# Kernel optimization log

Measured on AMD Instinct MI355X. Metric: run time of the kernel, lower is better.

The kernel has to match this reference:

```python
import jax, jax.numpy as jnp
import numpy as np

H = 16   # num_heads
D = 16   # key_dim == output_dim (required by the module's reshape)
F = 64   # input feature dim


def setup_inputs() -> dict:
    key = jax.random.key(0)
    ks = jax.random.split(key, 8)
    B, N, Kn = 4, 4096, 32
    scale = 1.0 / np.sqrt(F)
    return {
        "inp": jax.random.normal(ks[0], (B, N, Kn, F), dtype=jnp.float32),
        "query": jax.random.normal(ks[1], (B, N, F), dtype=jnp.float32),
        "Wq": jax.random.normal(ks[2], (F, H * D), dtype=jnp.float32) * scale,
        "bq": jnp.zeros((H * D,), dtype=jnp.float32),
        "Wk": jax.random.normal(ks[3], (F, H * D), dtype=jnp.float32) * scale,
        "bk": jnp.zeros((H * D,), dtype=jnp.float32),
        "Wv": jax.random.normal(ks[4], (F, H * D), dtype=jnp.float32) * scale,
        "bv": jnp.zeros((H * D,), dtype=jnp.float32),
    }


def reference(inp, query, Wq, bq, Wk, bk, Wv, bv):
    B, N, Kn, _ = inp.shape
    # Dense projections
    Q = query @ Wq + bq                    # [B, N, H*D]
    K = inp @ Wk + bk                      # [B, N, Kn, H*D]
    V = inp @ Wv + bv                      # [B, N, Kn, H*D]
    # Faithful reshape (plain reshape of last dims, as in the TF code)
    Q = Q.reshape(B, N, H, 1, D)           # query broadcast axis of size 1
    K = K.reshape(B, N, H, Kn, D)
    V = V.reshape(B, N, H, Kn, D)
    # scaled dot-product attention per point over its Kn neighbors
    w = jnp.einsum('bnhqd,bnhkd->bnhqk', Q, K) / jnp.sqrt(jnp.float32(D))
    w = jax.nn.softmax(w, axis=-1)         # [B, N, H, 1, Kn]
    out = jnp.einsum('bnhqk,bnhkd->bnhqd', w, V)  # [B, N, H, 1, D]
    return out.reshape(B, N, H * D)
```

## Files before the change

### kernel.cpp

```cpp
#include <hip/hip_runtime.h>

#define KN 32
#define FF 64
#define CC 256
#define KSTR 260
#define VST 36
#define VTOFF (KN * KSTR)
#define NITER 16
#define QSTRIDE 264
#define WSTRIDE 36


typedef __attribute__((ext_vector_type(8)))  short bf16x8;
typedef __attribute__((ext_vector_type(16))) float f32x16;
typedef __attribute__((ext_vector_type(4)))  float f32x4;

__device__ inline unsigned short f2bf(float f) {
    union { float f; unsigned u; } v; v.f = f;
    unsigned u = v.u + 0x7fffu + ((v.u >> 16) & 1u);
    return (unsigned short)(u >> 16);
}
__device__ inline unsigned cvt_pk_bf16(float a, float b) {
    unsigned r;
    asm("v_cvt_pk_bf16_f32 %0, %1, %2" : "=v"(r) : "v"(a), "v"(b));
    return r;
}
__device__ inline bf16x8 pack8(float4 a, float4 b) {
    union { bf16x8 v; unsigned u[4]; } r;
    r.u[0] = cvt_pk_bf16(a.x, a.y);  r.u[1] = cvt_pk_bf16(a.z, a.w);
    r.u[2] = cvt_pk_bf16(b.x, b.y);  r.u[3] = cvt_pk_bf16(b.z, b.w);
    return r.v;
}

__device__ inline void lds_barrier() {
    asm volatile("s_waitcnt lgkmcnt(0)" ::: "memory");
    __builtin_amdgcn_s_barrier();
}

__global__ __launch_bounds__(256, 2)
void attn_one(const float* __restrict__ inp,
              const float* __restrict__ query,
              const float* __restrict__ Wq,
              const float* __restrict__ bq,
              const float* __restrict__ Wk,
              const float* __restrict__ bk,
              const float* __restrict__ Wv,
              const float* __restrict__ bv,
              float* __restrict__ out, int nPoints)
{
    __shared__ float kvS[KN * KSTR + CC * VST];
    __shared__ unsigned short qAllS[NITER * QSTRIDE];
    __shared__ float wS[16 * WSTRIDE];

    const int tid  = threadIdx.x;
    const int wave = tid >> 6;
    const int L    = tid & 63;
    const int Lm   = L & 31;
    const int Lh   = L >> 5;
    const int h    = tid >> 4;
    const int d    = tid & 15;
    const int bid  = blockIdx.x;
    const int grid = gridDim.x;

    float* qIn = kvS;
    {
        const int i  = tid >> 4;
        const int f4 = (tid & 15) * 4;
        const int p  = bid + i * grid;
        if (p < nPoints)
            *(float4*)(qIn + i * 68 + f4) =
                *(const float4*)(query + (size_t)p * FF + f4);
    }

    float4 pf[8];
    {
        const float* arow = inp + (size_t)bid * (KN * FF) + Lm * FF + Lh * 8;
#pragma unroll
        for (int s = 0; s < 4; ++s) {
            pf[2 * s]     = *(const float4*)(arow + s * 16);
            pf[2 * s + 1] = *(const float4*)(arow + s * 16 + 4);
        }
    }

    bf16x8 Bf[4][4];
#pragma unroll
    for (int t = 0; t < 4; ++t) {
        const float* W  = (t < 2) ? Wk : Wv;
        const int ch    = (2 * wave + (t & 1)) * 32 + Lm;
#pragma unroll
        for (int s = 0; s < 4; ++s) {
            union { bf16x8 v; unsigned u[4]; } r;
#pragma unroll
            for (int jj = 0; jj < 4; ++jj) {
                const int f = s * 16 + Lh * 8 + 2 * jj;
                r.u[jj] = cvt_pk_bf16(W[(size_t)f * CC + ch], W[(size_t)(f + 1) * CC + ch]);
            }
            Bf[t][s] = r.v;
        }
    }
    float biasV[2];
    biasV[0] = bv[(2 * wave + 0) * 32 + Lm];
    biasV[1] = bv[(2 * wave + 1) * 32 + Lm];
    float4 bkK[2][4];
#pragma unroll
    for (int t = 0; t < 2; ++t)
#pragma unroll
        for (int g = 0; g < 4; ++g)
            bkK[t][g] = *(const float4*)(bk + (2 * wave + t) * 32 + 8 * g + 4 * Lh);

    const int nq = L & 15;
    const int kq = (L >> 4) * 8;
    bf16x8 Bq[4][2];
    float  bqv[4];
#pragma unroll
    for (int tt = 0; tt < 4; ++tt) {
        const int ch = wave * 64 + tt * 16 + nq;
        bqv[tt] = bq[ch];
#pragma unroll
        for (int s = 0; s < 2; ++s) {
            union { bf16x8 v; unsigned u[4]; } r;
#pragma unroll
            for (int jj = 0; jj < 4; ++jj) {
                const int f = s * 32 + kq + 2 * jj;
                r.u[jj] = cvt_pk_bf16(Wq[(size_t)f * CC + ch], Wq[(size_t)(f + 1) * CC + ch]);
            }
            Bq[tt][s] = r.v;
        }
    }

    __syncthreads();

    {
        bf16x8 Aq[2];
        const int im = L & 15;
#pragma unroll
        for (int s = 0; s < 2; ++s) {
            const float* qr = qIn + im * 68 + s * 32 + kq;
            Aq[s] = pack8(*(const float4*)qr, *(const float4*)(qr + 4));
        }
#pragma unroll
        for (int tt = 0; tt < 4; ++tt) {
            f32x4 qa = {bqv[tt], bqv[tt], bqv[tt], bqv[tt]};
#pragma unroll
            for (int s = 0; s < 2; ++s)
                qa = __builtin_amdgcn_mfma_f32_16x16x32_bf16(Aq[s], Bq[tt][s], qa, 0, 0, 0);
            const int ch = wave * 64 + tt * 16 + nq;
#pragma unroll
            for (int r = 0; r < 4; ++r) {
                const int ip = (L >> 4) * 4 + r;
                qAllS[ip * QSTRIDE + ch] = f2bf(qa[r] * 0.25f);
            }
        }
    }
    __syncthreads();

    const int sR = d & 7;
    const int j0 = 2 * h + (d >> 3);

    for (int it = 0, p = bid; p < nPoints; ++it, p += grid) {
        bf16x8 Af[4];
#pragma unroll
        for (int s = 0; s < 4; ++s) Af[s] = pack8(pf[2 * s], pf[2 * s + 1]);

        const int pn = p + grid;
        if (pn < nPoints) {
            const float* arow = inp + (size_t)pn * (KN * FF) + Lm * FF + Lh * 8;
#pragma unroll
            for (int s = 0; s < 4; ++s) {
                pf[2 * s]     = *(const float4*)(arow + s * 16);
                pf[2 * s + 1] = *(const float4*)(arow + s * 16 + 4);
            }
        }

        f32x16 acc[4];
#pragma unroll
        for (int t = 0; t < 2; ++t)
#pragma unroll
            for (int g = 0; g < 4; ++g)
#pragma unroll
                for (int e = 0; e < 4; ++e) acc[t][4 * g + e] = bkK[t][g][e];
#pragma unroll
        for (int t = 2; t < 4; ++t)
#pragma unroll
            for (int r = 0; r < 16; ++r) acc[t][r] = biasV[t - 2];

#pragma unroll
        for (int s = 0; s < 4; ++s) {
#pragma unroll
            for (int t = 0; t < 2; ++t)
                acc[t] = __builtin_amdgcn_mfma_f32_32x32x16_bf16(Bf[t][s], Af[s], acc[t], 0, 0, 0);
#pragma unroll
            for (int t = 2; t < 4; ++t)
                acc[t] = __builtin_amdgcn_mfma_f32_32x32x16_bf16(Af[s], Bf[t][s], acc[t], 0, 0, 0);
        }

#pragma unroll
        for (int t = 0; t < 2; ++t) {
            float* kr = kvS + Lm * KSTR + (2 * wave + t) * 32 + 4 * Lh;
#pragma unroll
            for (int g = 0; g < 4; ++g) {
                float4 vw = {acc[t][4 * g], acc[t][4 * g + 1], acc[t][4 * g + 2], acc[t][4 * g + 3]};
                *(float4*)(kr + 8 * g) = vw;
            }
        }
#pragma unroll
        for (int t = 2; t < 4; ++t) {
            const int col = (2 * wave + (t & 1)) * 32 + Lm;
            float* vr = kvS + VTOFF + col * VST + 4 * Lh;
#pragma unroll
            for (int g = 0; g < 4; ++g) {
                float4 vw = {acc[t][4 * g], acc[t][4 * g + 1], acc[t][4 * g + 2], acc[t][4 * g + 3]};
                *(float4*)(vr + 8 * g) = vw;
            }
        }

        const unsigned short* qp = qAllS + it * QSTRIDE + h * 16;
        uint4 qA = *(const uint4*)qp;
        uint4 qB = *(const uint4*)(qp + 8);

        lds_barrier();

        const float* kb = kvS + j0 * KSTR + sR * 32;
        float4 ck[8];
#pragma unroll
        for (int w = 0; w < 8; ++w)
            ck[w] = *(const float4*)(kb + 4 * w);

        union { uint4 v; unsigned u[4]; } ua, ub;
        ua.v = qA;  ub.v = qB;
        float qv[16];
#pragma unroll
        for (int j = 0; j < 4; ++j) {
            qv[2 * j]     = __uint_as_float(ua.u[j] << 16);
            qv[2 * j + 1] = __uint_as_float(ua.u[j] & 0xffff0000u);
            qv[8 + 2 * j]     = __uint_as_float(ub.u[j] << 16);
            qv[8 + 2 * j + 1] = __uint_as_float(ub.u[j] & 0xffff0000u);
        }

        float l0a = 0.f, l0b = 0.f, l1a = 0.f, l1b = 0.f;
#pragma unroll
        for (int i = 0; i < 16; i += 2) {
            l0a = fmaf(qv[i],     ck[i >> 2][i & 3],             l0a);
            l0b = fmaf(qv[i + 1], ck[(i + 1) >> 2][(i + 1) & 3], l0b);
            l1a = fmaf(qv[i],     ck[4 + (i >> 2)][i & 3],             l1a);
            l1b = fmaf(qv[i + 1], ck[4 + ((i + 1) >> 2)][(i + 1) & 3], l1b);
        }
        const float l0 = l0a + l0b;
        const float l1 = l1a + l1b;

        float m = fmaxf(l0, l1);
        m = fmaxf(m, __shfl_xor(m, 1));
        m = fmaxf(m, __shfl_xor(m, 2));
        m = fmaxf(m, __shfl_xor(m, 4));
        m = fmaxf(m, __shfl_xor(m, 8));
        float e0 = __expf(l0 - m), e1 = __expf(l1 - m);
        float s2 = e0 + e1;
        s2 += __shfl_xor(s2, 1);
        s2 += __shfl_xor(s2, 2);
        s2 += __shfl_xor(s2, 4);
        s2 += __shfl_xor(s2, 8);
        const float inv = 1.0f / s2;
        *(float2*)(wS + h * WSTRIDE + 2 * d) = make_float2(e0 * inv, e1 * inv);
        __builtin_amdgcn_wave_barrier();

        float4 wv[8];
#pragma unroll
        for (int g = 0; g < 8; ++g)
            wv[g] = *(const float4*)(wS + h * WSTRIDE + 4 * g);

        const float* Vb = kvS + VTOFF + d * VST + 2 * h;
        float o0 = 0.f, o1 = 0.f, o2 = 0.f, o3 = 0.f;
#pragma unroll
        for (int mI = 0; mI < 16; mI += 2) {
            const float2 va = *(const float2*)(Vb + (size_t)(16 * mI) * VST);
            const float2 vb = *(const float2*)(Vb + (size_t)(16 * (mI + 1)) * VST);
            o0 = fmaf(wv[mI >> 2][mI & 3],             va.x, o0);
            o1 = fmaf(wv[4 + (mI >> 2)][mI & 3],       va.y, o1);
            o2 = fmaf(wv[(mI + 1) >> 2][(mI + 1) & 3],       vb.x, o2);
            o3 = fmaf(wv[4 + ((mI + 1) >> 2)][(mI + 1) & 3], vb.y, o3);
        }
        out[(size_t)p * CC + tid] = (o0 + o1) + (o2 + o3);

        lds_barrier();
    }
}

extern "C" void kernel_launch(void* const* d_in, const int* in_sizes, int n_in,
                              void* d_out, int out_size, void* d_ws, size_t ws_size,
                              hipStream_t stream) {
    const float* inp   = (const float*)d_in[0];
    const float* query = (const float*)d_in[1];
    const float* Wq    = (const float*)d_in[2];
    const float* bq    = (const float*)d_in[3];
    const float* Wk    = (const float*)d_in[4];
    const float* bk    = (const float*)d_in[5];
    const float* Wv    = (const float*)d_in[6];
    const float* bv    = (const float*)d_in[7];
    float* out = (float*)d_out;

    const int nPoints = in_sizes[0] / (KN * FF);
    const int grid    = (nPoints + NITER - 1) / NITER;

    attn_one<<<grid, 256, 0, stream>>>(inp, query, Wq, bq, Wk, bk, Wv, bv,
                                       out, nPoints);
}
```

Measured before the change: 254.5 us.

## Store K/V tiles as bf16 in LDS, raise occupancy, prioritize MFMA

Projected K and V are now packed to bf16 before being written to shared memory, and the attention loop unpacks them on read. This halves the LDS footprint and the LDS traffic per point. The launch bound rises from 2 to 3 blocks per CU to use the freed LDS. The MFMA block is also wrapped in s_setprio to favour matrix issue. The risks are extra bf16 rounding error on K and V, and register pressure at the higher occupancy target.

```diff
diff --git a/kernel.cpp b/kernel.cpp
--- a/kernel.cpp
+++ b/kernel.cpp
@@ -3,9 +3,9 @@
 #define KN 32
 #define FF 64
 #define CC 256
-#define KSTR 260
-#define VST 36
-#define VTOFF (KN * KSTR)
+#define KSTRB 264
+#define VSTB 40
+#define VTOFFB (KN * KSTRB)
 #define NITER 16
 #define QSTRIDE 264
 #define WSTRIDE 36
@@ -31,13 +31,15 @@
     r.u[2] = cvt_pk_bf16(b.x, b.y);  r.u[3] = cvt_pk_bf16(b.z, b.w);
     return r.v;
 }
+__device__ inline float bflo(unsigned u) { return __uint_as_float(u << 16); }
+__device__ inline float bfhi(unsigned u) { return __uint_as_float(u & 0xffff0000u); }
 
 __device__ inline void lds_barrier() {
     asm volatile("s_waitcnt lgkmcnt(0)" ::: "memory");
     __builtin_amdgcn_s_barrier();
 }
 
-__global__ __launch_bounds__(256, 2)
+__global__ __launch_bounds__(256, 3)
 void attn_one(const float* __restrict__ inp,
               const float* __restrict__ query,
               const float* __restrict__ Wq,
@@ -48,7 +50,7 @@
               const float* __restrict__ bv,
               float* __restrict__ out, int nPoints)
 {
-    __shared__ float kvS[KN * KSTR + CC * VST];
+    __shared__ __align__(16) unsigned short kvS[KN * KSTRB + CC * VSTB];
     __shared__ unsigned short qAllS[NITER * QSTRIDE];
     __shared__ float wS[16 * WSTRIDE];
 
@@ -62,7 +64,7 @@
     const int bid  = blockIdx.x;
     const int grid = gridDim.x;
 
-    float* qIn = kvS;
+    float* qIn = (float*)kvS;
     {
         const int i  = tid >> 4;
         const int f4 = (tid & 15) * 4;
@@ -154,8 +156,9 @@
     }
     __syncthreads();
 
-    const int sR = d & 7;
-    const int j0 = 2 * h + (d >> 3);
+    const int sR  = d & 7;
+    const int j0  = 2 * h + (d >> 3);
+    const int vb0 = VTOFFB + 40 * d + 2 * h;
 
     for (int it = 0, p = bid; p < nPoints; ++it, p += grid) {
         bf16x8 Af[4];
@@ -184,6 +187,7 @@
 #pragma unroll
             for (int r = 0; r < 16; ++r) acc[t][r] = biasV[t - 2];
 
+        __builtin_amdgcn_s_setprio(1);
 #pragma unroll
         for (int s = 0; s < 4; ++s) {
 #pragma unroll
@@ -193,24 +197,27 @@
             for (int t = 2; t < 4; ++t)
                 acc[t] = __builtin_amdgcn_mfma_f32_32x32x16_bf16(Af[s], Bf[t][s], acc[t], 0, 0, 0);
         }
+        __builtin_amdgcn_s_setprio(0);
 
 #pragma unroll
         for (int t = 0; t < 2; ++t) {
-            float* kr = kvS + Lm * KSTR + (2 * wave + t) * 32 + 4 * Lh;
+            unsigned short* kr = kvS + Lm * KSTRB + (2 * wave + t) * 32 + 4 * Lh;
 #pragma unroll
             for (int g = 0; g < 4; ++g) {
-                float4 vw = {acc[t][4 * g], acc[t][4 * g + 1], acc[t][4 * g + 2], acc[t][4 * g + 3]};
-                *(float4*)(kr + 8 * g) = vw;
+                const unsigned p0 = cvt_pk_bf16(acc[t][4 * g],     acc[t][4 * g + 1]);
+                const unsigned p1 = cvt_pk_bf16(acc[t][4 * g + 2], acc[t][4 * g + 3]);
+                *(uint2*)(kr + 8 * g) = make_uint2(p0, p1);
             }
         }
 #pragma unroll
         for (int t = 2; t < 4; ++t) {
             const int col = (2 * wave + (t & 1)) * 32 + Lm;
-            float* vr = kvS + VTOFF + col * VST + 4 * Lh;
+            unsigned short* vr = kvS + VTOFFB + col * VSTB + 4 * Lh;
 #pragma unroll
             for (int g = 0; g < 4; ++g) {
-                float4 vw = {acc[t][4 * g], acc[t][4 * g + 1], acc[t][4 * g + 2], acc[t][4 * g + 3]};
-                *(float4*)(vr + 8 * g) = vw;
+                const unsigned p0 = cvt_pk_bf16(acc[t][4 * g],     acc[t][4 * g + 1]);
+                const unsigned p1 = cvt_pk_bf16(acc[t][4 * g + 2], acc[t][4 * g + 3]);
+                *(uint2*)(vr + 8 * g) = make_uint2(p0, p1);
             }
         }
 
@@ -220,30 +227,32 @@
 
         lds_barrier();
 
-        const float* kb = kvS + j0 * KSTR + sR * 32;
-        float4 ck[8];
-#pragma unroll
-        for (int w = 0; w < 8; ++w)
-            ck[w] = *(const float4*)(kb + 4 * w);
+        const unsigned short* kb = kvS + j0 * KSTRB + sR * 32;
+        union { uint4 v; unsigned u[4]; } ckb[4];
+#pragma unroll
+        for (int w = 0; w < 4; ++w)
+            ckb[w].v = *(const uint4*)(kb + 8 * w);
 
         union { uint4 v; unsigned u[4]; } ua, ub;
         ua.v = qA;  ub.v = qB;
         float qv[16];
 #pragma unroll
         for (int j = 0; j < 4; ++j) {
-            qv[2 * j]     = __uint_as_float(ua.u[j] << 16);
-            qv[2 * j + 1] = __uint_as_float(ua.u[j] & 0xffff0000u);
-            qv[8 + 2 * j]     = __uint_as_float(ub.u[j] << 16);
-            qv[8 + 2 * j + 1] = __uint_as_float(ub.u[j] & 0xffff0000u);
+            qv[2 * j]         = bflo(ua.u[j]);
+            qv[2 * j + 1]     = bfhi(ua.u[j]);
+            qv[8 + 2 * j]     = bflo(ub.u[j]);
+            qv[8 + 2 * j + 1] = bfhi(ub.u[j]);
         }
 
         float l0a = 0.f, l0b = 0.f, l1a = 0.f, l1b = 0.f;
 #pragma unroll
-        for (int i = 0; i < 16; i += 2) {
-            l0a = fmaf(qv[i],     ck[i >> 2][i & 3],             l0a);
-            l0b = fmaf(qv[i + 1], ck[(i + 1) >> 2][(i + 1) & 3], l0b);
-            l1a = fmaf(qv[i],     ck[4 + (i >> 2)][i & 3],             l1a);
-            l1b = fmaf(qv[i + 1], ck[4 + ((i + 1) >> 2)][(i + 1) & 3], l1b);
+        for (int dd = 0; dd < 8; ++dd) {
+            const unsigned u0 = ckb[dd >> 2].u[dd & 3];
+            const unsigned u1 = ckb[2 + (dd >> 2)].u[dd & 3];
+            l0a = fmaf(qv[2 * dd],     bflo(u0), l0a);
+            l0b = fmaf(qv[2 * dd + 1], bfhi(u0), l0b);
+            l1a = fmaf(qv[2 * dd],     bflo(u1), l1a);
+            l1b = fmaf(qv[2 * dd + 1], bfhi(u1), l1b);
         }
         const float l0 = l0a + l0b;
         const float l1 = l1a + l1b;
@@ -268,16 +277,15 @@
         for (int g = 0; g < 8; ++g)
             wv[g] = *(const float4*)(wS + h * WSTRIDE + 4 * g);
 
-        const float* Vb = kvS + VTOFF + d * VST + 2 * h;
         float o0 = 0.f, o1 = 0.f, o2 = 0.f, o3 = 0.f;
 #pragma unroll
         for (int mI = 0; mI < 16; mI += 2) {
-            const float2 va = *(const float2*)(Vb + (size_t)(16 * mI) * VST);
-            const float2 vb = *(const float2*)(Vb + (size_t)(16 * (mI + 1)) * VST);
-            o0 = fmaf(wv[mI >> 2][mI & 3],             va.x, o0);
-            o1 = fmaf(wv[4 + (mI >> 2)][mI & 3],       va.y, o1);
-            o2 = fmaf(wv[(mI + 1) >> 2][(mI + 1) & 3],       vb.x, o2);
-            o3 = fmaf(wv[4 + ((mI + 1) >> 2)][(mI + 1) & 3], vb.y, o3);
+            const unsigned va = *(const unsigned*)(kvS + vb0 + 640 * mI);
+            const unsigned vb = *(const unsigned*)(kvS + vb0 + 640 * (mI + 1));
+            o0 = fmaf(wv[mI >> 2][mI & 3],                   bflo(va), o0);
+            o1 = fmaf(wv[4 + (mI >> 2)][mI & 3],             bfhi(va), o1);
+            o2 = fmaf(wv[(mI + 1) >> 2][(mI + 1) & 3],       bflo(vb), o2);
+            o3 = fmaf(wv[4 + ((mI + 1) >> 2)][(mI + 1) & 3], bfhi(vb), o3);
         }
         out[(size_t)p * CC + tid] = (o0 + o1) + (o2 + o3);
 
```

Result: slower. 518.8 us (+103.8%).
